# Kernel tuning notes

Hardware: AMD Instinct MI355X
Metric: run time of the kernel (lower is better)

## Reference

```python
import jax, jax.numpy as jnp
import numpy as np
from jax import lax

GAMMA = 0.99

def setup_inputs() -> dict:
    key = jax.random.key(0)
    ks = jax.random.split(key, 6)
    B, T, D = 2048, 512, 16
    return {
        "Q": jax.random.normal(ks[0], (B, T, D), dtype=jnp.float32),
        "expected_target_Q": jax.random.normal(ks[1], (B, T, D), dtype=jnp.float32),
        "target_Q": jax.random.normal(ks[2], (B, T, D), dtype=jnp.float32),
        "rewards": jax.random.normal(ks[3], (B, T, D), dtype=jnp.float32),
        "target_policy_probs": jax.random.normal(ks[4], (B, T, D), dtype=jnp.float32),
        "behaviour_policy_probs": jax.random.normal(ks[5], (B, T), dtype=jnp.float32),
    }


def _q_ret(expected_target_Q, target_Q, rewards, target_policy_probs, behaviour_policy_probs):
    # importance weights c = exp(min(log_pi - log_b, 0)), shape [B, T, D]
    c = jnp.exp(jnp.minimum(target_policy_probs - behaviour_policy_probs[..., None], 0.0))
    T = target_Q.shape[1]
    # time-major slices for steps j = 0..T-2
    tm = lambda x: jnp.swapaxes(x, 0, 1)  # [T, B, D] -> scan over leading axis
    xs = (tm(rewards[:, : T - 1]), tm(expected_target_Q[:, 1:]),
          tm(c[:, 1:]), tm(target_Q[:, 1:]))

    def step(carry, x):
        r, e, cw, tq = x
        q = r + GAMMA * (e + cw * (carry - tq))
        return q, q

    # reverse scan: Q_ret[j] depends on Q_ret[j+1]; init carry is target_Q[:, -1]
    _, q_ret = lax.scan(step, target_Q[:, -1], xs, reverse=True)
    return jnp.swapaxes(q_ret, 0, 1)  # [B, T-1, D] == Q_ret[:, :-1]


def reference(Q, expected_target_Q, target_Q, rewards, target_policy_probs, behaviour_policy_probs):
    q_ret = lax.stop_gradient(
        _q_ret(expected_target_Q, target_Q, rewards, target_policy_probs, behaviour_policy_probs))
    return jnp.mean((Q[:, :-1] - q_ret) ** 2)
```

## Files before the change

### kernel.cpp

```cpp
#include <hip/hip_runtime.h>


constexpr int B  = 2048;
constexpr int T  = 512;
constexpr int D  = 16;
constexpr int NC = 16;
constexpr int CS = 32;
constexpr int BPB = 4;
constexpr int SQ = B * (D / 4);
constexpr float GAMMA = 0.99f;
constexpr float LOG2E = 1.44269504088896340736f;

constexpr int QSEG  = CS * D + 16;
constexpr int BGSEG = CS * D * 2 + 16;
constexpr int LDS_FLOATS = BPB * QSEG + BPB * BGSEG;

__device__ __forceinline__ void load_lds16(const float* g, float* l) {
    __builtin_amdgcn_global_load_lds(
        (const __attribute__((address_space(1))) unsigned int*)g,
        (__attribute__((address_space(3))) unsigned int*)l, 16, 0, 0);
}

struct ScanState { float alpha, beta, P, S, W; };

template<int N>
__device__ __forceinline__ void scan_batch(const float* __restrict__ sBG,
                                           const float* __restrict__ sQ,
                                           const int i0, ScanState& st) {
    float2 bg[N];
    float  q[N];
    #pragma unroll
    for (int j = 0; j < N; ++j) {
        bg[j] = *(const float2*)(sBG + 32 * (i0 + j));
        q[j]  = sQ[(i0 + j) * D];
    }
    #pragma unroll
    for (int j = N - 1; j >= 0; --j) {
        const float g = bg[j].y;
        st.alpha = fmaf(g, st.alpha, bg[j].x);
        st.beta  = g * st.beta;
        const float u = q[j] - st.alpha;
        st.P = fmaf(u, u, st.P);
        st.S = fmaf(u, st.beta, st.S);
        st.W = fmaf(st.beta, st.beta, st.W);
    }
}

__global__ __launch_bounds__(64, 2) void retrace_phase1(
    const float* __restrict__ Q,
    const float* __restrict__ eQ,
    const float* __restrict__ tQ,
    const float* __restrict__ rw,
    const float* __restrict__ tpp,
    const float* __restrict__ bpp,
    float* __restrict__ ws)
{
    __shared__ __align__(16) float lds[LDS_FLOATS];
    float* lQ  = lds;
    float* lBG = lds + BPB * QSEG;

    const int tid = threadIdx.x;
    const int bid = blockIdx.x;
    const int k   = bid & (NC - 1);
    const int b0  = (bid >> 4) * BPB;
    const int t0  = k * CS;

    const bool last = (k == NC - 1);
    const int rows = last ? (CS - 1) : CS;
    const int n4   = rows * (D / 4);

    float4 ev4[BPB][2], tq4[BPB][2], tp4[BPB][2], rv4[BPB][2];
    float  bpv[BPB][2];
    #pragma unroll
    for (int bl = 0; bl < BPB; ++bl) {
        const size_t rb = ((size_t)(b0 + bl) * T + t0) * (D / 4);
        const float4* ge = (const float4*)eQ  + rb + (D / 4);
        const float4* gt = (const float4*)tQ  + rb + (D / 4);
        const float4* gp = (const float4*)tpp + rb + (D / 4);
        const float4* gr = (const float4*)rw  + rb;
        const float*  gb = bpp + (size_t)(b0 + bl) * T + t0 + 1;
        #pragma unroll
        for (int h = 0; h < 2; ++h) {
            const int off = tid + 64 * h;
            if (off < n4) {
                ev4[bl][h] = ge[off];
                tq4[bl][h] = gt[off];
                tp4[bl][h] = gp[off];
                rv4[bl][h] = gr[off];
                bpv[bl][h] = gb[off >> 2];
            }
        }
    }

    #pragma unroll
    for (int bl = 0; bl < BPB; ++bl) {
        const float* gq = Q + ((size_t)(b0 + bl) * T + t0) * D;
        float* l = lQ + bl * QSEG;
        #pragma unroll
        for (int h = 0; h < 2; ++h) {
            const int off = tid + 64 * h;
            if (off < n4) load_lds16(gq + (size_t)off * 4, l + (size_t)off * 4);
        }
    }

    #pragma unroll
    for (int bl = 0; bl < BPB; ++bl) {
        float* lbg = lBG + bl * BGSEG;
        #pragma unroll
        for (int h = 0; h < 2; ++h) {
            const int off = tid + 64 * h;
            if (off < n4) {
                const float* e = (const float*)&ev4[bl][h];
                const float* t = (const float*)&tq4[bl][h];
                const float* p = (const float*)&tp4[bl][h];
                const float* r = (const float*)&rv4[bl][h];
                const float bp = bpv[bl][h];
                float bg[8];
                #pragma unroll
                for (int j = 0; j < 4; ++j) {
                    const float cw = __builtin_exp2f(fminf(p[j] - bp, 0.f) * LOG2E);
                    const float g  = GAMMA * cw;
                    bg[2 * j]     = fmaf(-g, t[j], fmaf(GAMMA, e[j], r[j]));
                    bg[2 * j + 1] = g;
                }
                float4* dst = (float4*)(lbg + (size_t)off * 8);
                dst[0] = make_float4(bg[0], bg[1], bg[2], bg[3]);
                dst[1] = make_float4(bg[4], bg[5], bg[6], bg[7]);
            }
        }
    }

    __syncthreads();

    const int bl = tid >> 4;
    const int d  = tid & 15;
    const float* sQ  = lQ  + bl * QSEG + d;
    const float* sBG = lBG + bl * BGSEG + 2 * d;

    ScanState st = {0.f, 1.f, 0.f, 0.f, 0.f};
    if (last) scan_batch<15>(sBG, sQ, 16, st);
    else      scan_batch<16>(sBG, sQ, 16, st);
    scan_batch<16>(sBG, sQ, 0, st);

    const size_t AS = (size_t)NC * SQ * 4;
    const size_t o  = ((size_t)k * SQ + (size_t)b0 * 4) * 4 + tid;
    ws[0 * AS + o] = st.alpha;
    ws[1 * AS + o] = st.beta;
    ws[2 * AS + o] = st.P;
    ws[3 * AS + o] = st.S;
    ws[4 * AS + o] = st.W;
}

__global__ __launch_bounds__(64) void retrace_phase2(
    const float* __restrict__ tQ,
    const float4* __restrict__ ws,
    float* __restrict__ out)
{
    const int s  = blockIdx.x * blockDim.x + threadIdx.x;
    const int b  = s >> 2;
    const int dq = s & 3;

    const float4* wsA = ws;
    const float4* wsM = ws + (size_t)NC * SQ;
    const float4* wsP = ws + (size_t)2 * NC * SQ;
    const float4* wsS = ws + (size_t)3 * NC * SQ;
    const float4* wsW = ws + (size_t)4 * NC * SQ;

    float4 c4 = ((const float4*)tQ)[((size_t)b * T + (T - 1)) * 4 + dq];
    float* c = (float*)&c4;
    float loss[4] = {0.f, 0.f, 0.f, 0.f};

    #pragma unroll
    for (int k = NC - 1; k >= 0; --k) {
        const size_t o = (size_t)k * SQ + s;
        const float4 A4 = wsA[o], M4 = wsM[o], P4 = wsP[o], S4 = wsS[o], W4 = wsW[o];
        const float* A = (const float*)&A4;
        const float* M = (const float*)&M4;
        const float* P = (const float*)&P4;
        const float* S = (const float*)&S4;
        const float* W = (const float*)&W4;
        #pragma unroll
        for (int i = 0; i < 4; ++i) {
            loss[i] += fmaf(c[i], fmaf(W[i], c[i], -2.f * S[i]), P[i]);
            c[i] = fmaf(M[i], c[i], A[i]);
        }
    }

    float acc = (loss[0] + loss[1]) + (loss[2] + loss[3]);
    #pragma unroll
    for (int off = 32; off > 0; off >>= 1)
        acc += __shfl_down(acc, off, 64);

    if (threadIdx.x == 0) {
        constexpr float inv_count = 1.0f / ((float)B * (float)(T - 1) * (float)D);
        atomicAdd(out, acc * inv_count);
    }
}

extern "C" void kernel_launch(void* const* d_in, const int* in_sizes, int n_in,
                              void* d_out, int out_size, void* d_ws, size_t ws_size,
                              hipStream_t stream) {
    const float* Q   = (const float*)d_in[0];
    const float* eQ  = (const float*)d_in[1];
    const float* tQ  = (const float*)d_in[2];
    const float* rw  = (const float*)d_in[3];
    const float* tpp = (const float*)d_in[4];
    const float* bpp = (const float*)d_in[5];
    float* out = (float*)d_out;
    float* ws = (float*)d_ws;

    hipMemsetAsync(out, 0, sizeof(float), stream);

    retrace_phase1<<<dim3(B / BPB * NC), dim3(64), 0, stream>>>(
        Q, eQ, tQ, rw, tpp, bpp, ws);

    retrace_phase2<<<dim3(SQ / 64), dim3(64), 0, stream>>>(tQ, (const float4*)ws, out);
}
```

Measured before the change: 302.8 us.

## Fuse chunk scan and combine into one persistent-per-batch pipelined kernel

Replaces the two-kernel chunked scan (per-chunk statistics written to workspace, then combined) with a single kernel where each block walks all time chunks of its batch rows in reverse. It software-pipelines global loads into registers and double-buffers LDS staging, combining chunk results on the fly. This removes workspace traffic and the second launch, but cuts the grid to one wave per four batch rows. That greatly reduces parallelism and memory-latency hiding and raises register pressure.

```diff
diff --git a/kernel.cpp b/kernel.cpp
--- a/kernel.cpp
+++ b/kernel.cpp
@@ -7,21 +7,83 @@
 constexpr int NC = 16;
 constexpr int CS = 32;
 constexpr int BPB = 4;
-constexpr int SQ = B * (D / 4);
 constexpr float GAMMA = 0.99f;
 constexpr float LOG2E = 1.44269504088896340736f;
 
 constexpr int QSEG  = CS * D + 16;
 constexpr int BGSEG = CS * D * 2 + 16;
-constexpr int LDS_FLOATS = BPB * QSEG + BPB * BGSEG;
-
-__device__ __forceinline__ void load_lds16(const float* g, float* l) {
-    __builtin_amdgcn_global_load_lds(
-        (const __attribute__((address_space(1))) unsigned int*)g,
-        (__attribute__((address_space(3))) unsigned int*)l, 16, 0, 0);
-}
+constexpr int BUFSZ = BPB * (QSEG + BGSEG);
+constexpr int LDS_FLOATS = 2 * BUFSZ;
 
 struct ScanState { float alpha, beta, P, S, W; };
+
+struct Raw {
+    float4 ev[BPB][2], tq[BPB][2], tp[BPB][2], rv[BPB][2], qv[BPB][2];
+    float  bp[BPB][2];
+};
+
+template<bool GUARD>
+__device__ __forceinline__ void issue_loads(
+    const int k, Raw& R, const int b0, const int tid,
+    const float* __restrict__ Q,  const float* __restrict__ eQ,
+    const float* __restrict__ tQ, const float* __restrict__ rw,
+    const float* __restrict__ tpp, const float* __restrict__ bpp)
+{
+    const int t0 = k * CS;
+    #pragma unroll
+    for (int bl = 0; bl < BPB; ++bl) {
+        const size_t rb = ((size_t)(b0 + bl) * T + t0) * (D / 4);
+        const float4* gq = (const float4*)Q   + rb;
+        const float4* ge = (const float4*)eQ  + rb + (D / 4);
+        const float4* gt = (const float4*)tQ  + rb + (D / 4);
+        const float4* gp = (const float4*)tpp + rb + (D / 4);
+        const float4* gr = (const float4*)rw  + rb;
+        const float*  gb = bpp + (size_t)(b0 + bl) * T + t0 + 1;
+        #pragma unroll
+        for (int h = 0; h < 2; ++h) {
+            const int off = tid + 64 * h;
+            if (!GUARD || off < (CS - 1) * (D / 4)) {
+                R.qv[bl][h] = gq[off];
+                R.ev[bl][h] = ge[off];
+                R.tq[bl][h] = gt[off];
+                R.tp[bl][h] = gp[off];
+                R.rv[bl][h] = gr[off];
+                R.bp[bl][h] = gb[off >> 2];
+            }
+        }
+    }
+}
+
+__device__ __forceinline__ void stage(const Raw& R, float* __restrict__ buf,
+                                      const int tid)
+{
+    float* lQ  = buf;
+    float* lBG = buf + BPB * QSEG;
+    #pragma unroll
+    for (int bl = 0; bl < BPB; ++bl) {
+        #pragma unroll
+        for (int h = 0; h < 2; ++h) {
+            const int off = tid + 64 * h;
+            const float* e = (const float*)&R.ev[bl][h];
+            const float* t = (const float*)&R.tq[bl][h];
+            const float* p = (const float*)&R.tp[bl][h];
+            const float* r = (const float*)&R.rv[bl][h];
+            const float bp = R.bp[bl][h];
+            float bg[8];
+            #pragma unroll
+            for (int j = 0; j < 4; ++j) {
+                const float cw = __builtin_exp2f(fminf(p[j] - bp, 0.f) * LOG2E);
+                const float g  = GAMMA * cw;
+                bg[2 * j]     = fmaf(-g, t[j], fmaf(GAMMA, e[j], r[j]));
+                bg[2 * j + 1] = g;
+            }
+            float4* dst = (float4*)(lBG + bl * BGSEG + (size_t)off * 8);
+            dst[0] = make_float4(bg[0], bg[1], bg[2], bg[3]);
+            dst[1] = make_float4(bg[4], bg[5], bg[6], bg[7]);
+            *(float4*)(lQ + bl * QSEG + (size_t)off * 4) = R.qv[bl][h];
+        }
+    }
+}
 
 template<int N>
 __device__ __forceinline__ void scan_batch(const float* __restrict__ sBG,
@@ -46,152 +108,75 @@
     }
 }
 
-__global__ __launch_bounds__(64, 2) void retrace_phase1(
+template<bool LAST>
+__device__ __forceinline__ ScanState scan_chunk(const float* __restrict__ buf,
+                                                const int tid) {
+    const int bl = tid >> 4;
+    const int d  = tid & 15;
+    const float* sQ  = buf + bl * QSEG + d;
+    const float* sBG = buf + BPB * QSEG + bl * BGSEG + 2 * d;
+    ScanState st = {0.f, 1.f, 0.f, 0.f, 0.f};
+    if (LAST) scan_batch<15>(sBG, sQ, 16, st);
+    else      scan_batch<16>(sBG, sQ, 16, st);
+    scan_batch<16>(sBG, sQ, 0, st);
+    return st;
+}
+
+#define COMBINE() do { \
+    loss = fmaf(c, fmaf(st.W, c, -2.f * st.S), st.P) + loss; \
+    c = fmaf(st.beta, c, st.alpha); \
+} while (0)
+
+__global__ __launch_bounds__(64, 1) void retrace_fused(
     const float* __restrict__ Q,
     const float* __restrict__ eQ,
     const float* __restrict__ tQ,
     const float* __restrict__ rw,
     const float* __restrict__ tpp,
     const float* __restrict__ bpp,
-    float* __restrict__ ws)
+    float* __restrict__ out)
 {
     __shared__ __align__(16) float lds[LDS_FLOATS];
-    float* lQ  = lds;
-    float* lBG = lds + BPB * QSEG;
+    float* buf0 = lds;
+    float* buf1 = lds + BUFSZ;
 
     const int tid = threadIdx.x;
-    const int bid = blockIdx.x;
-    const int k   = bid & (NC - 1);
-    const int b0  = (bid >> 4) * BPB;
-    const int t0  = k * CS;
-
-    const bool last = (k == NC - 1);
-    const int rows = last ? (CS - 1) : CS;
-    const int n4   = rows * (D / 4);
-
-    float4 ev4[BPB][2], tq4[BPB][2], tp4[BPB][2], rv4[BPB][2];
-    float  bpv[BPB][2];
-    #pragma unroll
-    for (int bl = 0; bl < BPB; ++bl) {
-        const size_t rb = ((size_t)(b0 + bl) * T + t0) * (D / 4);
-        const float4* ge = (const float4*)eQ  + rb + (D / 4);
-        const float4* gt = (const float4*)tQ  + rb + (D / 4);
-        const float4* gp = (const float4*)tpp + rb + (D / 4);
-        const float4* gr = (const float4*)rw  + rb;
-        const float*  gb = bpp + (size_t)(b0 + bl) * T + t0 + 1;
-        #pragma unroll
-        for (int h = 0; h < 2; ++h) {
-            const int off = tid + 64 * h;
-            if (off < n4) {
-                ev4[bl][h] = ge[off];
-                tq4[bl][h] = gt[off];
-                tp4[bl][h] = gp[off];
-                rv4[bl][h] = gr[off];
-                bpv[bl][h] = gb[off >> 2];
-            }
-        }
-    }
-
-    #pragma unroll
-    for (int bl = 0; bl < BPB; ++bl) {
-        const float* gq = Q + ((size_t)(b0 + bl) * T + t0) * D;
-        float* l = lQ + bl * QSEG;
-        #pragma unroll
-        for (int h = 0; h < 2; ++h) {
-            const int off = tid + 64 * h;
-            if (off < n4) load_lds16(gq + (size_t)off * 4, l + (size_t)off * 4);
-        }
-    }
-
-    #pragma unroll
-    for (int bl = 0; bl < BPB; ++bl) {
-        float* lbg = lBG + bl * BGSEG;
-        #pragma unroll
-        for (int h = 0; h < 2; ++h) {
-            const int off = tid + 64 * h;
-            if (off < n4) {
-                const float* e = (const float*)&ev4[bl][h];
-                const float* t = (const float*)&tq4[bl][h];
-                const float* p = (const float*)&tp4[bl][h];
-                const float* r = (const float*)&rv4[bl][h];
-                const float bp = bpv[bl][h];
-                float bg[8];
-                #pragma unroll
-                for (int j = 0; j < 4; ++j) {
-                    const float cw = __builtin_exp2f(fminf(p[j] - bp, 0.f) * LOG2E);
-                    const float g  = GAMMA * cw;
-                    bg[2 * j]     = fmaf(-g, t[j], fmaf(GAMMA, e[j], r[j]));
-                    bg[2 * j + 1] = g;
-                }
-                float4* dst = (float4*)(lbg + (size_t)off * 8);
-                dst[0] = make_float4(bg[0], bg[1], bg[2], bg[3]);
-                dst[1] = make_float4(bg[4], bg[5], bg[6], bg[7]);
-            }
-        }
-    }
-
-    __syncthreads();
-
-    const int bl = tid >> 4;
-    const int d  = tid & 15;
-    const float* sQ  = lQ  + bl * QSEG + d;
-    const float* sBG = lBG + bl * BGSEG + 2 * d;
-
-    ScanState st = {0.f, 1.f, 0.f, 0.f, 0.f};
-    if (last) scan_batch<15>(sBG, sQ, 16, st);
-    else      scan_batch<16>(sBG, sQ, 16, st);
-    scan_batch<16>(sBG, sQ, 0, st);
-
-    const size_t AS = (size_t)NC * SQ * 4;
-    const size_t o  = ((size_t)k * SQ + (size_t)b0 * 4) * 4 + tid;
-    ws[0 * AS + o] = st.alpha;
-    ws[1 * AS + o] = st.beta;
-    ws[2 * AS + o] = st.P;
-    ws[3 * AS + o] = st.S;
-    ws[4 * AS + o] = st.W;
-}
-
-__global__ __launch_bounds__(64) void retrace_phase2(
-    const float* __restrict__ tQ,
-    const float4* __restrict__ ws,
-    float* __restrict__ out)
-{
-    const int s  = blockIdx.x * blockDim.x + threadIdx.x;
-    const int b  = s >> 2;
-    const int dq = s & 3;
-
-    const float4* wsA = ws;
-    const float4* wsM = ws + (size_t)NC * SQ;
-    const float4* wsP = ws + (size_t)2 * NC * SQ;
-    const float4* wsS = ws + (size_t)3 * NC * SQ;
-    const float4* wsW = ws + (size_t)4 * NC * SQ;
-
-    float4 c4 = ((const float4*)tQ)[((size_t)b * T + (T - 1)) * 4 + dq];
-    float* c = (float*)&c4;
-    float loss[4] = {0.f, 0.f, 0.f, 0.f};
-
-    #pragma unroll
-    for (int k = NC - 1; k >= 0; --k) {
-        const size_t o = (size_t)k * SQ + s;
-        const float4 A4 = wsA[o], M4 = wsM[o], P4 = wsP[o], S4 = wsS[o], W4 = wsW[o];
-        const float* A = (const float*)&A4;
-        const float* M = (const float*)&M4;
-        const float* P = (const float*)&P4;
-        const float* S = (const float*)&S4;
-        const float* W = (const float*)&W4;
-        #pragma unroll
-        for (int i = 0; i < 4; ++i) {
-            loss[i] += fmaf(c[i], fmaf(W[i], c[i], -2.f * S[i]), P[i]);
-            c[i] = fmaf(M[i], c[i], A[i]);
-        }
-    }
-
-    float acc = (loss[0] + loss[1]) + (loss[2] + loss[3]);
+    const int b0  = blockIdx.x * BPB;
+
+    const int bl_l = tid >> 4, d_l = tid & 15;
+    float c = tQ[((size_t)(b0 + bl_l) * T + (T - 1)) * D + d_l];
+    float loss = 0.f;
+
+    Raw R0, R1;
+
+    issue_loads<true >(15, R1, b0, tid, Q, eQ, tQ, rw, tpp, bpp);
+    issue_loads<false>(14, R0, b0, tid, Q, eQ, tQ, rw, tpp, bpp);
+    stage(R1, buf1, tid);
+    issue_loads<false>(13, R1, b0, tid, Q, eQ, tQ, rw, tpp, bpp);
+    ScanState st = scan_chunk<true>(buf1, tid);
+    COMBINE();
+    stage(R0, buf0, tid);
+
+    for (int j = 14; j >= 2; j -= 2) {
+        issue_loads<false>(j - 2, R0, b0, tid, Q, eQ, tQ, rw, tpp, bpp);
+        st = scan_chunk<false>(buf0, tid);
+        COMBINE();
+        stage(R1, buf1, tid);
+        if (j >= 4)
+            issue_loads<false>(j - 3, R1, b0, tid, Q, eQ, tQ, rw, tpp, bpp);
+        st = scan_chunk<false>(buf1, tid);
+        COMBINE();
+        stage(R0, buf0, tid);
+    }
+
+    st = scan_chunk<false>(buf0, tid);
+    loss = fmaf(c, fmaf(st.W, c, -2.f * st.S), st.P) + loss;
+
+    float acc = loss;
     #pragma unroll
     for (int off = 32; off > 0; off >>= 1)
         acc += __shfl_down(acc, off, 64);
-
-    if (threadIdx.x == 0) {
+    if (tid == 0) {
         constexpr float inv_count = 1.0f / ((float)B * (float)(T - 1) * (float)D);
         atomicAdd(out, acc * inv_count);
     }
@@ -207,12 +192,10 @@
     const float* tpp = (const float*)d_in[4];
     const float* bpp = (const float*)d_in[5];
     float* out = (float*)d_out;
-    float* ws = (float*)d_ws;
+    (void)d_ws; (void)ws_size;
 
     hipMemsetAsync(out, 0, sizeof(float), stream);
 
-    retrace_phase1<<<dim3(B / BPB * NC), dim3(64), 0, stream>>>(
-        Q, eQ, tQ, rw, tpp, bpp, ws);
-
-    retrace_phase2<<<dim3(SQ / 64), dim3(64), 0, stream>>>(tQ, (const float4*)ws, out);
-}
+    retrace_fused<<<dim3(B / BPB), dim3(64), 0, stream>>>(
+        Q, eQ, tQ, rw, tpp, bpp, out);
+}
```

Result: no change. 302.3 us (-0.2%).
